# Performance work log

Hardware: AMD Instinct MI355X
Metric: run time of the kernel (lower is better)

The kernel has to match this reference:

```python
import jax, jax.numpy as jnp
import numpy as np

H = 16      # n_heads
D = 1024    # d_model
DK = D // H # head dim


def setup_inputs() -> dict:
    key = jax.random.key(0)
    ks = jax.random.split(key, 11)
    B, S = 4, 2048
    std = 1.0 / np.sqrt(D)
    inp = {
        "query": jax.random.normal(ks[0], (B, S, D), jnp.float32),
        "key": jax.random.normal(ks[1], (B, S, D), jnp.float32),
        "value": jax.random.normal(ks[2], (B, S, D), jnp.float32),
        "Wq": jax.random.normal(ks[3], (D, D), jnp.float32) * std,
        "bq": jnp.zeros((D,), jnp.float32),
        "Wk": jax.random.normal(ks[4], (D, D), jnp.float32) * std,
        "bk": jnp.zeros((D,), jnp.float32),
        "Wv": jax.random.normal(ks[5], (D, D), jnp.float32) * std,
        "bv": jnp.zeros((D,), jnp.float32),
        "Wo": jax.random.normal(ks[6], (D, D), jnp.float32) * std,
        "bo": jnp.zeros((D,), jnp.float32),
    }
    return inp


def reference(query, key, value, Wq, bq, Wk, bk, Wv, bv, Wo, bo):
    B, S, _ = query.shape
    # QKV projections (nn.Linear), then split heads: [B, S, H, DK]
    q = (query @ Wq + bq).reshape(B, S, H, DK)
    k = (key @ Wk + bk).reshape(B, S, H, DK)
    v = (value @ Wv + bv).reshape(B, S, H, DK)
    # Memory-efficient attention computes exactly softmax(QK^T/sqrt(dk))V
    scale = 1.0 / np.sqrt(DK).astype(np.float32)
    scores = jnp.einsum("bqhd,bkhd->bhqk", q, k) * scale  # [B, H, S, S]
    attn = jax.nn.softmax(scores, axis=-1)
    x = jnp.einsum("bhqk,bkhd->bqhd", attn, v)            # [B, S, H, DK]
    x = x.reshape(B, S, H * DK)
    return x @ Wo + bo
```

## Files before the change

### kernel.cpp

```cpp
#include <hip/hip_runtime.h>
#include <hip/hip_bf16.h>

typedef short short8 __attribute__((ext_vector_type(8)));
typedef float f32x4 __attribute__((ext_vector_type(4)));
typedef float f32x16 __attribute__((ext_vector_type(16)));
typedef unsigned short u16;
typedef unsigned int u32;

#define HD 16
#define DMODEL 1024
#define DKH 64
#define SEQ 2048
#define QSCALE 0.18033688f

typedef const __attribute__((address_space(1))) void gvoid;
typedef __attribute__((address_space(3))) void lvoid;

__device__ inline u16 f2bf(float f) {
  unsigned int x = __builtin_bit_cast(unsigned int, f);
  unsigned int r = (x + 0x7fffu + ((x >> 16) & 1u)) >> 16;
  return (u16)r;
}

__device__ inline float fexp2(float x) {
#if __has_builtin(__builtin_amdgcn_exp2f)
  return __builtin_amdgcn_exp2f(x);
#else
  return __expf(x * 0.69314718f);
#endif
}

__device__ inline u32 cvtpk(float lo, float hi_) {
  u32 r;
  asm("v_cvt_pk_bf16_f32 %0, %1, %2" : "=v"(r) : "v"(lo), "v"(hi_));
  return r;
}

__device__ inline f32x4 mfma16(short8 a, short8 b, f32x4 c) {
  return __builtin_amdgcn_mfma_f32_16x16x32_bf16(a, b, c, 0, 0, 0);
}
__device__ inline f32x16 mfma32(short8 a, short8 b, f32x16 c) {
  return __builtin_amdgcn_mfma_f32_32x32x16_bf16(a, b, c, 0, 0, 0);
}

__global__ __launch_bounds__(256) void wt_kernel(const float* __restrict__ W0,
                                                 const float* __restrict__ W1,
                                                 const float* __restrict__ W2,
                                                 const float* __restrict__ W3,
                                                 u16* __restrict__ T) {
  __shared__ float tile[64][65];
  const float* W = blockIdx.z == 0 ? W0 : blockIdx.z == 1 ? W1 : blockIdx.z == 2 ? W2 : W3;
  u16* out = T + (size_t)blockIdx.z * DMODEL * DMODEL;
  int n0 = blockIdx.x * 64, k0 = blockIdx.y * 64;
  int tx = threadIdx.x & 63, ty = threadIdx.x >> 6;
  for (int i = 0; i < 16; i++) {
    int r = ty + i * 4;
    tile[r][tx] = W[(size_t)(k0 + r) * DMODEL + n0 + tx];
  }
  __syncthreads();
  for (int i = 0; i < 16; i++) {
    int r = ty + i * 4;
    out[(size_t)(n0 + r) * DMODEL + k0 + tx] = f2bf(tile[tx][r]);
  }
}

__global__ __launch_bounds__(256, 2) void gemm_qkv(const float* __restrict__ q,
                                                   const float* __restrict__ k,
                                                   const float* __restrict__ v,
                                                   const u16* __restrict__ WT,
                                                   const float* __restrict__ bq,
                                                   const float* __restrict__ bk,
                                                   const float* __restrict__ bv,
                                                   u16* __restrict__ Qb,
                                                   u16* __restrict__ Kb,
                                                   u16* __restrict__ Vtb) {
  __shared__ u16 As[2][128 * 64];
  __shared__ u16 Bs[2][128 * 64];
  const int b = blockIdx.x;
  const int xcd = b & 7, slot = b >> 3;
  const int nidx = slot & 7, pl = slot >> 3;
  const int pg = xcd * 24 + pl;
  const int z = pg >> 6, by = pg & 63;

  const float* A = z == 0 ? q : z == 1 ? k : v;
  const u16* Bt = WT + (size_t)z * DMODEL * DMODEL;
  const float* bias = z == 0 ? bq : z == 1 ? bk : bv;
  u16* Cv = z == 0 ? Qb : z == 1 ? Kb : Vtb;
  const float scale = z == 0 ? QSCALE : 1.0f;
  const bool vtrans = (z == 2);

  const int m0 = by * 128, n0 = nidx * 128;
  const int tid = threadIdx.x;
  const int lane = tid & 63, wid = tid >> 6;
  const int g = lane >> 4, c = lane & 15;
  const int wr = (wid >> 1) * 64, wc = (wid & 1) * 64;

  const int trow = tid >> 3;
  const int tcolb = (tid & 7) << 4;
  const int swr = (c & 7) << 4;
  f32x4 acc[4][4] = {};
  float4 ar[4][2];

#define STAGE_B(buf, kk0)                                                          \
  _Pragma("unroll") for (int p = 0; p < 4; ++p) {                                  \
    const int row = p * 32 + trow;                                                 \
    const int scol = tcolb ^ ((row & 7) << 4);                                     \
    __builtin_amdgcn_global_load_lds(                                              \
        (gvoid*)((const char*)Bt + ((size_t)(n0 + row) * DMODEL + (kk0)) * 2 + scol), \
        (lvoid*)((char*)&Bs[buf][0] + row * 128 + tcolb), 16, 0, 0);               \
  }
#define LOAD_A(kk0)                                                                \
  _Pragma("unroll") for (int p = 0; p < 4; ++p) {                                  \
    const int row = p * 32 + trow;                                                 \
    const float* src = A + (size_t)(m0 + row) * DMODEL + (kk0) + (tid & 7) * 8;    \
    ar[p][0] = *(const float4*)src;                                                \
    ar[p][1] = *(const float4*)(src + 4);                                          \
  }
#define CVT_WRITE_A(buf)                                                           \
  _Pragma("unroll") for (int p = 0; p < 4; ++p) {                                  \
    const int row = p * 32 + trow;                                                 \
    u32 tmp[4] = {cvtpk(ar[p][0].x, ar[p][0].y), cvtpk(ar[p][0].z, ar[p][0].w),    \
                  cvtpk(ar[p][1].x, ar[p][1].y), cvtpk(ar[p][1].z, ar[p][1].w)};   \
    *(uint4*)((char*)&As[buf][0] + row * 128 + (tcolb ^ ((row & 7) << 4))) = *(uint4*)tmp; \
  }

  STAGE_B(0, 0);
  LOAD_A(0);
  CVT_WRITE_A(0);
  STAGE_B(1, 64);
  LOAD_A(64);
  __syncthreads();

  for (int t = 0; t < 16; ++t) {
    const int cur = t & 1;
    short8 af[4][2], bfr[4][2];
#pragma unroll
    for (int kk = 0; kk < 2; ++kk) {
#pragma unroll
      for (int mi = 0; mi < 4; ++mi)
        af[mi][kk] = *(const short8*)((const char*)&As[cur][0] + (wr + mi * 16 + c) * 128 + ((kk * 64 + g * 16) ^ swr));
#pragma unroll
      for (int ni = 0; ni < 4; ++ni)
        bfr[ni][kk] = *(const short8*)((const char*)&Bs[cur][0] + (wc + ni * 16 + c) * 128 + ((kk * 64 + g * 16) ^ swr));
    }
    if (t < 15) CVT_WRITE_A(cur ^ 1);
    if (t < 14) LOAD_A((t + 2) * 64);
    __builtin_amdgcn_s_setprio(1);
#pragma unroll
    for (int kk = 0; kk < 2; ++kk)
#pragma unroll
      for (int mi = 0; mi < 4; ++mi)
#pragma unroll
        for (int ni = 0; ni < 4; ++ni)
          acc[mi][ni] = mfma16(af[mi][kk], bfr[ni][kk], acc[mi][ni]);
    __builtin_amdgcn_s_setprio(0);
    __syncthreads();
    if (t < 14) STAGE_B(cur, (t + 2) * 64);
  }
#undef STAGE_B
#undef LOAD_A
#undef CVT_WRITE_A

  for (int ni = 0; ni < 4; ++ni) {
    const int colg = n0 + wc + ni * 16 + c;
    const float bv_ = bias[colg];
    for (int mi = 0; mi < 4; ++mi) {
      const int rowb = m0 + wr + mi * 16 + g * 4;
      const int bb = rowb >> 11, s = rowb & 2047;
      const int h = colg >> 6, dk = colg & 63;
      if (!vtrans) {
        const size_t base = ((size_t)(bb * HD + h)) * SEQ;
        for (int j = 0; j < 4; ++j)
          Cv[(base + s + j) * DKH + dk] = f2bf((acc[mi][ni][j] + bv_) * scale);
      } else {
        const size_t base = ((size_t)(bb * HD + h) * DKH + dk) * SEQ + s;
        ushort4 u;
        u.x = f2bf(acc[mi][ni][0] + bv_);
        u.y = f2bf(acc[mi][ni][1] + bv_);
        u.z = f2bf(acc[mi][ni][2] + bv_);
        u.w = f2bf(acc[mi][ni][3] + bv_);
        *(ushort4*)(&Cv[base]) = u;
      }
    }
  }
}

__global__ __launch_bounds__(256, 2) void gemm_out(const u16* __restrict__ A,
                                                   const u16* __restrict__ Bt,
                                                   const float* __restrict__ bias,
                                                   float* __restrict__ C) {
  __shared__ u16 As[2][128 * 64];
  __shared__ u16 Bs[2][128 * 64];
  const int b = blockIdx.x;
  const int xcd = b & 7, slot = b >> 3;
  const int nidx = slot & 7, pl = slot >> 3;
  const int by = xcd * 8 + pl;

  const int m0 = by * 128, n0 = nidx * 128;
  const int tid = threadIdx.x;
  const int lane = tid & 63, wid = tid >> 6;
  const int g = lane >> 4, c = lane & 15;
  const int wr = (wid >> 1) * 64, wc = (wid & 1) * 64;

  const int trow = tid >> 3;
  const int tcolb = (tid & 7) << 4;
  const int swr = (c & 7) << 4;
  f32x4 acc[4][4] = {};

#define STAGE_AB(buf, kk0)                                                         \
  _Pragma("unroll") for (int p = 0; p < 4; ++p) {                                  \
    const int row = p * 32 + trow;                                                 \
    const int scol = tcolb ^ ((row & 7) << 4);                                     \
    __builtin_amdgcn_global_load_lds(                                              \
        (gvoid*)((const char*)A + ((size_t)(m0 + row) * DMODEL + (kk0)) * 2 + scol), \
        (lvoid*)((char*)&As[buf][0] + row * 128 + tcolb), 16, 0, 0);               \
    __builtin_amdgcn_global_load_lds(                                              \
        (gvoid*)((const char*)Bt + ((size_t)(n0 + row) * DMODEL + (kk0)) * 2 + scol), \
        (lvoid*)((char*)&Bs[buf][0] + row * 128 + tcolb), 16, 0, 0);               \
  }

  STAGE_AB(0, 0);
  STAGE_AB(1, 64);
  __syncthreads();

  for (int t = 0; t < 16; ++t) {
    const int cur = t & 1;
    short8 af[4][2], bfr[4][2];
#pragma unroll
    for (int kk = 0; kk < 2; ++kk) {
#pragma unroll
      for (int mi = 0; mi < 4; ++mi)
        af[mi][kk] = *(const short8*)((const char*)&As[cur][0] + (wr + mi * 16 + c) * 128 + ((kk * 64 + g * 16) ^ swr));
#pragma unroll
      for (int ni = 0; ni < 4; ++ni)
        bfr[ni][kk] = *(const short8*)((const char*)&Bs[cur][0] + (wc + ni * 16 + c) * 128 + ((kk * 64 + g * 16) ^ swr));
    }
    __builtin_amdgcn_s_setprio(1);
#pragma unroll
    for (int kk = 0; kk < 2; ++kk)
#pragma unroll
      for (int mi = 0; mi < 4; ++mi)
#pragma unroll
        for (int ni = 0; ni < 4; ++ni)
          acc[mi][ni] = mfma16(af[mi][kk], bfr[ni][kk], acc[mi][ni]);
    __builtin_amdgcn_s_setprio(0);
    __syncthreads();
    if (t < 14) STAGE_AB(cur, (t + 2) * 64);
  }
#undef STAGE_AB

  for (int ni = 0; ni < 4; ++ni) {
    const int colg = n0 + wc + ni * 16 + c;
    const float bv = bias[colg];
    for (int mi = 0; mi < 4; ++mi) {
      const int rowb = m0 + wr + mi * 16 + g * 4;
      for (int j = 0; j < 4; ++j)
        C[(size_t)(rowb + j) * DMODEL + colg] = acc[mi][ni][j] + bv;
    }
  }
}

__global__ __launch_bounds__(256, 4) void attn_kernel(const u16* __restrict__ Q,
                                                      const u16* __restrict__ K,
                                                      const u16* __restrict__ Vt,
                                                      u16* __restrict__ X) {
  __shared__ char ldsmem[2][2][8192];
  const int tid = threadIdx.x;
  const int lane = tid & 63, wid = tid >> 6;
  const int c5 = lane & 31, hi = lane >> 5;

  const int blk = blockIdx.x;
  const int work = (blk & 7) * 128 + (blk >> 3);
  const int qt = work & 15, bh = work >> 4;

  const int q0 = qt * 128 + wid * 32;
  const u16* qb = Q + (size_t)bh * SEQ * DKH;
  const char* kbB = (const char*)(K + (size_t)bh * SEQ * DKH);
  const char* vbB = (const char*)(Vt + (size_t)bh * DKH * SEQ);

  short8 qf[4];
#pragma unroll
  for (int ks = 0; ks < 4; ++ks)
    qf[ks] = *(const short8*)(qb + (size_t)(q0 + c5) * DKH + ks * 16 + hi * 8);

  const int srow = tid >> 3;
  const int scolb = (tid & 7) << 4;
  const int scol = scolb ^ ((srow & 7) << 4);

  const int fswz = (c5 & 7) << 4;
  int cofs[4];
#pragma unroll
  for (int ks = 0; ks < 4; ++ks) cofs[ks] = ((ks * 32 + hi * 16) ^ fswz);

  f32x16 oacc[2] = {};
  float mrun = -1e30f, lrun = 0.f;

#pragma unroll
  for (int r32 = 0; r32 < 64; r32 += 32) {
    __builtin_amdgcn_global_load_lds(
        (gvoid*)(kbB + (size_t)(r32 + srow) * 128 + scol),
        (lvoid*)(&ldsmem[0][0][(r32 + srow) * 128 + scolb]), 16, 0, 0);
    __builtin_amdgcn_global_load_lds(
        (gvoid*)(vbB + (size_t)(r32 + srow) * (SEQ * 2) + scol),
        (lvoid*)(&ldsmem[0][1][(r32 + srow) * 128 + scolb]), 16, 0, 0);
  }
  __syncthreads();

#pragma unroll 2
  for (int t = 0; t < 32; ++t) {
    const int buf = t & 1;
    if (t < 31) {
      const size_t kv1 = (size_t)(t + 1) * 64;
#pragma unroll
      for (int r32 = 0; r32 < 64; r32 += 32) {
        __builtin_amdgcn_global_load_lds(
            (gvoid*)(kbB + (kv1 + r32 + srow) * 128 + scol),
            (lvoid*)(&ldsmem[buf ^ 1][0][(r32 + srow) * 128 + scolb]), 16, 0, 0);
        __builtin_amdgcn_global_load_lds(
            (gvoid*)(vbB + (size_t)(r32 + srow) * (SEQ * 2) + kv1 * 2 + scol),
            (lvoid*)(&ldsmem[buf ^ 1][1][(r32 + srow) * 128 + scolb]), 16, 0, 0);
      }
    }

    const char* bK = &ldsmem[buf][0][0];
    const char* bV = &ldsmem[buf][1][0];

    f32x16 sacc[2] = {};
#pragma unroll
    for (int kt = 0; kt < 2; ++kt) {
      short8 kf[4];
#pragma unroll
      for (int ks = 0; ks < 4; ++ks)
        kf[ks] = *(const short8*)(bK + (kt * 32 + c5) * 128 + cofs[ks]);
#pragma unroll
      for (int ks = 0; ks < 4; ++ks)
        sacc[kt] = mfma32(kf[ks], qf[ks], sacc[kt]);
    }

    float pm = sacc[0][0];
#pragma unroll
    for (int kt = 0; kt < 2; ++kt)
#pragma unroll
      for (int r = 0; r < 16; ++r) pm = fmaxf(pm, sacc[kt][r]);
    pm = fmaxf(pm, __shfl_xor(pm, 32, 64));

    if (!__all(pm <= mrun + 11.5f)) {
      float mnew = fmaxf(mrun, pm);
      float a = fexp2(mrun - mnew);
      mrun = mnew;
      lrun *= a;
#pragma unroll
      for (int r = 0; r < 16; ++r) {
        float ar = __shfl(a, (r & 3) + 8 * (r >> 2) + 4 * hi, 64);
        oacc[0][r] *= ar;
        oacc[1][r] *= ar;
      }
    }
    float rs = 0.f;
#pragma unroll
    for (int kt = 0; kt < 2; ++kt)
#pragma unroll
      for (int r = 0; r < 16; ++r) {
        float p = fexp2(sacc[kt][r] - mrun);
        sacc[kt][r] = p;
        rs += p;
      }
    rs += __shfl_xor(rs, 32, 64);
    lrun += rs;

    u32 W[2][8], Xw[2][8];
#pragma unroll
    for (int kt = 0; kt < 2; ++kt)
#pragma unroll
      for (int j = 0; j < 8; ++j) {
        W[kt][j] = cvtpk(sacc[kt][2 * j], sacc[kt][2 * j + 1]);
        Xw[kt][j] = __shfl_xor(W[kt][j], 32, 64);
      }
    short8 pa[4];
#pragma unroll
    for (int ks = 0; ks < 4; ++ks) {
      const int kt = ks >> 1, l4 = (ks & 1) * 4;
      u32 m0 = hi ? Xw[kt][l4 + 2] : W[kt][l4 + 0];
      u32 m1 = hi ? Xw[kt][l4 + 3] : W[kt][l4 + 1];
      u32 m2 = hi ? W[kt][l4 + 2] : Xw[kt][l4 + 0];
      u32 m3 = hi ? W[kt][l4 + 3] : Xw[kt][l4 + 1];
      u32 tmp[4] = {m0, m1, m2, m3};
      pa[ks] = *(const short8*)tmp;
    }

    short8 vf[2][4];
#pragma unroll
    for (int dkt = 0; dkt < 2; ++dkt)
#pragma unroll
      for (int ks = 0; ks < 4; ++ks)
        vf[dkt][ks] = *(const short8*)(bV + (dkt * 32 + c5) * 128 + cofs[ks]);
#pragma unroll
    for (int ks = 0; ks < 4; ++ks)
#pragma unroll
      for (int dkt = 0; dkt < 2; ++dkt)
        oacc[dkt] = mfma32(pa[ks], vf[dkt][ks], oacc[dkt]);

    __syncthreads();
  }

  const int b = bh >> 4, h = bh & 15;
  const float inv = 1.0f / lrun;
#pragma unroll
  for (int r = 0; r < 16; ++r) {
    const int qrow = (r & 3) + 8 * (r >> 2) + 4 * hi;
    const float linv = __shfl(inv, qrow, 64);
    const size_t rowbase = ((size_t)(b * SEQ) + q0 + qrow) * DMODEL + h * DKH;
#pragma unroll
    for (int dkt = 0; dkt < 2; ++dkt)
      X[rowbase + dkt * 32 + c5] = f2bf(oacc[dkt][r] * linv);
  }
}

extern "C" void kernel_launch(void* const* d_in, const int* in_sizes, int n_in,
                              void* d_out, int out_size, void* d_ws, size_t ws_size,
                              hipStream_t stream) {
  (void)in_sizes; (void)n_in; (void)out_size; (void)ws_size;
  const float* query = (const float*)d_in[0];
  const float* key   = (const float*)d_in[1];
  const float* value = (const float*)d_in[2];
  const float* Wq = (const float*)d_in[3];
  const float* bq = (const float*)d_in[4];
  const float* Wk = (const float*)d_in[5];
  const float* bk = (const float*)d_in[6];
  const float* Wv = (const float*)d_in[7];
  const float* bv = (const float*)d_in[8];
  const float* Wo = (const float*)d_in[9];
  const float* bo = (const float*)d_in[10];
  float* out = (float*)d_out;

  char* ws = (char*)d_ws;
  const size_t MB = 1024 * 1024;
  u16* WT  = (u16*)ws;
  u16* Qb  = (u16*)(ws + 8 * MB);
  u16* Kb  = (u16*)(ws + 24 * MB);
  u16* Vtb = (u16*)(ws + 40 * MB);
  u16* Xb  = (u16*)(ws + 56 * MB);

  wt_kernel<<<dim3(16, 16, 4), 256, 0, stream>>>(Wq, Wk, Wv, Wo, WT);
  gemm_qkv<<<dim3(1536), 256, 0, stream>>>(query, key, value, WT, bq, bk, bv, Qb, Kb, Vtb);
  attn_kernel<<<dim3(1024), 256, 0, stream>>>(Qb, Kb, Vtb, Xb);
  gemm_out<<<dim3(512), 256, 0, stream>>>(Xb, WT + 3 * 1048576, bo, out);
}
```

Measured before the change: 203.1 us.

## Pre-convert QKV activations to bf16 in a fused prep kernel

Adds a prep kernel that converts the fp32 query/key/value activations to bf16 in a separate pass, merged into the same launch as the weight transpose. The QKV GEMM can then load A tiles through async global-to-LDS loads like B, with no register staging and no in-loop conversion. The cost is an extra full read and write of the activations through HBM (96MB read, 48MB written) and a larger workspace. The Xb buffer is moved to alias the now-dead Qf region.

```diff
diff --git a/kernel.cpp b/kernel.cpp
--- a/kernel.cpp
+++ b/kernel.cpp
@@ -43,30 +43,52 @@
   return __builtin_amdgcn_mfma_f32_32x32x16_bf16(a, b, c, 0, 0, 0);
 }
 
-__global__ __launch_bounds__(256) void wt_kernel(const float* __restrict__ W0,
-                                                 const float* __restrict__ W1,
-                                                 const float* __restrict__ W2,
-                                                 const float* __restrict__ W3,
-                                                 u16* __restrict__ T) {
-  __shared__ float tile[64][65];
-  const float* W = blockIdx.z == 0 ? W0 : blockIdx.z == 1 ? W1 : blockIdx.z == 2 ? W2 : W3;
-  u16* out = T + (size_t)blockIdx.z * DMODEL * DMODEL;
-  int n0 = blockIdx.x * 64, k0 = blockIdx.y * 64;
-  int tx = threadIdx.x & 63, ty = threadIdx.x >> 6;
-  for (int i = 0; i < 16; i++) {
-    int r = ty + i * 4;
-    tile[r][tx] = W[(size_t)(k0 + r) * DMODEL + n0 + tx];
-  }
-  __syncthreads();
-  for (int i = 0; i < 16; i++) {
-    int r = ty + i * 4;
-    out[(size_t)(n0 + r) * DMODEL + k0 + tx] = f2bf(tile[tx][r]);
-  }
-}
-
-__global__ __launch_bounds__(256, 2) void gemm_qkv(const float* __restrict__ q,
+__global__ __launch_bounds__(256) void prep_kernel(const float* __restrict__ q,
                                                    const float* __restrict__ k,
                                                    const float* __restrict__ v,
+                                                   const float* __restrict__ W0,
+                                                   const float* __restrict__ W1,
+                                                   const float* __restrict__ W2,
+                                                   const float* __restrict__ W3,
+                                                   u16* __restrict__ Qf,
+                                                   u16* __restrict__ Kf,
+                                                   u16* __restrict__ Vf,
+                                                   u16* __restrict__ WT) {
+  const int z = blockIdx.z;
+  if (z < 3) {
+    const float* src = z == 0 ? q : z == 1 ? k : v;
+    u16* dst = z == 0 ? Qf : z == 1 ? Kf : Vf;
+    const int nthr = gridDim.x * 256;
+    for (size_t i = blockIdx.x * 256 + threadIdx.x; i < (size_t)(SEQ * 4) * DMODEL / 8; i += nthr) {
+      const float4 a0 = *(const float4*)(src + i * 8);
+      const float4 a1 = *(const float4*)(src + i * 8 + 4);
+      u32 tmp[4] = {cvtpk(a0.x, a0.y), cvtpk(a0.z, a0.w),
+                    cvtpk(a1.x, a1.y), cvtpk(a1.z, a1.w)};
+      *(uint4*)(dst + i * 8) = *(uint4*)tmp;
+    }
+  } else {
+    __shared__ float tile[64][65];
+    const int b = blockIdx.x;
+    const int w = b >> 8;
+    const int n0 = (b & 15) * 64, k0 = ((b >> 4) & 15) * 64;
+    const float* W = w == 0 ? W0 : w == 1 ? W1 : w == 2 ? W2 : W3;
+    u16* out = WT + (size_t)w * DMODEL * DMODEL;
+    int tx = threadIdx.x & 63, ty = threadIdx.x >> 6;
+    for (int i = 0; i < 16; i++) {
+      int r = ty + i * 4;
+      tile[r][tx] = W[(size_t)(k0 + r) * DMODEL + n0 + tx];
+    }
+    __syncthreads();
+    for (int i = 0; i < 16; i++) {
+      int r = ty + i * 4;
+      out[(size_t)(n0 + r) * DMODEL + k0 + tx] = f2bf(tile[tx][r]);
+    }
+  }
+}
+
+__global__ __launch_bounds__(256, 2) void gemm_qkv(const u16* __restrict__ Qf,
+                                                   const u16* __restrict__ Kf,
+                                                   const u16* __restrict__ Vf,
                                                    const u16* __restrict__ WT,
                                                    const float* __restrict__ bq,
                                                    const float* __restrict__ bk,
@@ -82,7 +104,7 @@
   const int pg = xcd * 24 + pl;
   const int z = pg >> 6, by = pg & 63;
 
-  const float* A = z == 0 ? q : z == 1 ? k : v;
+  const u16* A = z == 0 ? Qf : z == 1 ? Kf : Vf;
   const u16* Bt = WT + (size_t)z * DMODEL * DMODEL;
   const float* bias = z == 0 ? bq : z == 1 ? bk : bv;
   u16* Cv = z == 0 ? Qb : z == 1 ? Kb : Vtb;
@@ -99,36 +121,21 @@
   const int tcolb = (tid & 7) << 4;
   const int swr = (c & 7) << 4;
   f32x4 acc[4][4] = {};
-  float4 ar[4][2];
-
-#define STAGE_B(buf, kk0)                                                          \
-  _Pragma("unroll") for (int p = 0; p < 4; ++p) {                                  \
-    const int row = p * 32 + trow;                                                 \
-    const int scol = tcolb ^ ((row & 7) << 4);                                     \
-    __builtin_amdgcn_global_load_lds(                                              \
+
+#define STAGE_AB(buf, kk0)                                                            \
+  _Pragma("unroll") for (int p = 0; p < 4; ++p) {                                     \
+    const int row = p * 32 + trow;                                                    \
+    const int scol = tcolb ^ ((row & 7) << 4);                                        \
+    __builtin_amdgcn_global_load_lds(                                                 \
+        (gvoid*)((const char*)A + ((size_t)(m0 + row) * DMODEL + (kk0)) * 2 + scol),  \
+        (lvoid*)((char*)&As[buf][0] + row * 128 + tcolb), 16, 0, 0);                  \
+    __builtin_amdgcn_global_load_lds(                                                 \
         (gvoid*)((const char*)Bt + ((size_t)(n0 + row) * DMODEL + (kk0)) * 2 + scol), \
-        (lvoid*)((char*)&Bs[buf][0] + row * 128 + tcolb), 16, 0, 0);               \
-  }
-#define LOAD_A(kk0)                                                                \
-  _Pragma("unroll") for (int p = 0; p < 4; ++p) {                                  \
-    const int row = p * 32 + trow;                                                 \
-    const float* src = A + (size_t)(m0 + row) * DMODEL + (kk0) + (tid & 7) * 8;    \
-    ar[p][0] = *(const float4*)src;                                                \
-    ar[p][1] = *(const float4*)(src + 4);                                          \
-  }
-#define CVT_WRITE_A(buf)                                                           \
-  _Pragma("unroll") for (int p = 0; p < 4; ++p) {                                  \
-    const int row = p * 32 + trow;                                                 \
-    u32 tmp[4] = {cvtpk(ar[p][0].x, ar[p][0].y), cvtpk(ar[p][0].z, ar[p][0].w),    \
-                  cvtpk(ar[p][1].x, ar[p][1].y), cvtpk(ar[p][1].z, ar[p][1].w)};   \
-    *(uint4*)((char*)&As[buf][0] + row * 128 + (tcolb ^ ((row & 7) << 4))) = *(uint4*)tmp; \
-  }
-
-  STAGE_B(0, 0);
-  LOAD_A(0);
-  CVT_WRITE_A(0);
-  STAGE_B(1, 64);
-  LOAD_A(64);
+        (lvoid*)((char*)&Bs[buf][0] + row * 128 + tcolb), 16, 0, 0);                  \
+  }
+
+  STAGE_AB(0, 0);
+  STAGE_AB(1, 64);
   __syncthreads();
 
   for (int t = 0; t < 16; ++t) {
@@ -143,8 +150,6 @@
       for (int ni = 0; ni < 4; ++ni)
         bfr[ni][kk] = *(const short8*)((const char*)&Bs[cur][0] + (wc + ni * 16 + c) * 128 + ((kk * 64 + g * 16) ^ swr));
     }
-    if (t < 15) CVT_WRITE_A(cur ^ 1);
-    if (t < 14) LOAD_A((t + 2) * 64);
     __builtin_amdgcn_s_setprio(1);
 #pragma unroll
     for (int kk = 0; kk < 2; ++kk)
@@ -155,11 +160,9 @@
           acc[mi][ni] = mfma16(af[mi][kk], bfr[ni][kk], acc[mi][ni]);
     __builtin_amdgcn_s_setprio(0);
     __syncthreads();
-    if (t < 14) STAGE_B(cur, (t + 2) * 64);
-  }
-#undef STAGE_B
-#undef LOAD_A
-#undef CVT_WRITE_A
+    if (t < 14) STAGE_AB(cur, (t + 2) * 64);
+  }
+#undef STAGE_AB
 
   for (int ni = 0; ni < 4; ++ni) {
     const int colg = n0 + wc + ni * 16 + c;
@@ -207,16 +210,16 @@
   const int swr = (c & 7) << 4;
   f32x4 acc[4][4] = {};
 
-#define STAGE_AB(buf, kk0)                                                         \
-  _Pragma("unroll") for (int p = 0; p < 4; ++p) {                                  \
-    const int row = p * 32 + trow;                                                 \
-    const int scol = tcolb ^ ((row & 7) << 4);                                     \
-    __builtin_amdgcn_global_load_lds(                                              \
-        (gvoid*)((const char*)A + ((size_t)(m0 + row) * DMODEL + (kk0)) * 2 + scol), \
-        (lvoid*)((char*)&As[buf][0] + row * 128 + tcolb), 16, 0, 0);               \
-    __builtin_amdgcn_global_load_lds(                                              \
+#define STAGE_AB(buf, kk0)                                                            \
+  _Pragma("unroll") for (int p = 0; p < 4; ++p) {                                     \
+    const int row = p * 32 + trow;                                                    \
+    const int scol = tcolb ^ ((row & 7) << 4);                                        \
+    __builtin_amdgcn_global_load_lds(                                                 \
+        (gvoid*)((const char*)A + ((size_t)(m0 + row) * DMODEL + (kk0)) * 2 + scol),  \
+        (lvoid*)((char*)&As[buf][0] + row * 128 + tcolb), 16, 0, 0);                  \
+    __builtin_amdgcn_global_load_lds(                                                 \
         (gvoid*)((const char*)Bt + ((size_t)(n0 + row) * DMODEL + (kk0)) * 2 + scol), \
-        (lvoid*)((char*)&Bs[buf][0] + row * 128 + tcolb), 16, 0, 0);               \
+        (lvoid*)((char*)&Bs[buf][0] + row * 128 + tcolb), 16, 0, 0);                  \
   }
 
   STAGE_AB(0, 0);
@@ -436,13 +439,17 @@
   char* ws = (char*)d_ws;
   const size_t MB = 1024 * 1024;
   u16* WT  = (u16*)ws;
-  u16* Qb  = (u16*)(ws + 8 * MB);
-  u16* Kb  = (u16*)(ws + 24 * MB);
-  u16* Vtb = (u16*)(ws + 40 * MB);
-  u16* Xb  = (u16*)(ws + 56 * MB);
-
-  wt_kernel<<<dim3(16, 16, 4), 256, 0, stream>>>(Wq, Wk, Wv, Wo, WT);
-  gemm_qkv<<<dim3(1536), 256, 0, stream>>>(query, key, value, WT, bq, bk, bv, Qb, Kb, Vtb);
+  u16* Qf  = (u16*)(ws + 8 * MB);
+  u16* Kf  = (u16*)(ws + 24 * MB);
+  u16* Vf  = (u16*)(ws + 40 * MB);
+  u16* Qb  = (u16*)(ws + 56 * MB);
+  u16* Kb  = (u16*)(ws + 72 * MB);
+  u16* Vtb = (u16*)(ws + 88 * MB);
+  u16* Xb  = (u16*)(ws + 8 * MB);
+
+  prep_kernel<<<dim3(1024, 1, 4), 256, 0, stream>>>(query, key, value, Wq, Wk, Wv, Wo,
+                                                    Qf, Kf, Vf, WT);
+  gemm_qkv<<<dim3(1536), 256, 0, stream>>>(Qf, Kf, Vf, WT, bq, bk, bv, Qb, Kb, Vtb);
   attn_kernel<<<dim3(1024), 256, 0, stream>>>(Qb, Kb, Vtb, Xb);
   gemm_out<<<dim3(512), 256, 0, stream>>>(Xb, WT + 3 * 1048576, bo, out);
 }
```

Result: slower. 207.5 us (+2.2%).
